# Kernel optimization log

Hardware: AMD Instinct MI355X
Metric: run time of the kernel (lower is better)

## Reference

```python
import jax, jax.numpy as jnp
import numpy as np

N, E, FX, H, B = 50000, 800000, 64, 64, 8
EPS = 1e-5


def _bn(h, gamma, beta):
    # BatchNorm1d in training mode: batch statistics, biased variance
    mu = h.mean(axis=0)
    var = ((h - mu) ** 2).mean(axis=0)
    return (h - mu) * jax.lax.rsqrt(var + EPS) * gamma + beta


def setup_inputs() -> dict:
    key = jax.random.key(0)
    ks = jax.random.split(key, 10)
    s = 0.05
    inp = {
        "x": jax.random.normal(ks[0], (N, FX), jnp.float32),
        "edge_index": jax.random.randint(ks[1], (2, E), 0, N),
        "edge_attr": jax.random.normal(ks[2], (E, H), jnp.float32),
        "u": jnp.zeros((1,), jnp.float32),
        "batch": jax.random.randint(ks[3], (E,), 0, B),
        # message_function params: Linear(FX+H->H), BN(H), Linear(H->H)
        "w1m": jax.random.normal(ks[4], (FX + H, H), jnp.float32) * s,
        "b1m": jnp.zeros((H,), jnp.float32),
        "gamma_m": jnp.ones((H,), jnp.float32),
        "beta_m": jnp.zeros((H,), jnp.float32),
        "w2m": jax.random.normal(ks[5], (H, H), jnp.float32) * s,
        "b2m": jnp.zeros((H,), jnp.float32),
        # node_mlp params: Linear(FX+H->H), BN(H), Linear(H->H)
        "w1n": jax.random.normal(ks[6], (FX + H, H), jnp.float32) * s,
        "b1n": jnp.zeros((H,), jnp.float32),
        "gamma_n": jnp.ones((H,), jnp.float32),
        "beta_n": jnp.zeros((H,), jnp.float32),
        "w2n": jax.random.normal(ks[7], (H, H), jnp.float32) * s,
        "b2n": jnp.zeros((H,), jnp.float32),
    }
    return inp


def reference(x, edge_index, edge_attr, u, batch,
              w1m, b1m, gamma_m, beta_m, w2m, b2m,
              w1n, b1n, gamma_n, beta_n, w2n, b2n):
    send_idx, rec_idx = edge_index[0], edge_index[1]
    n = x.shape[0]
    # gather sender node features, concat with edge features: [E, FX+H]
    m = jnp.concatenate([x[send_idx], edge_attr], axis=1)
    # message MLP: Linear -> BN -> ReLU -> Linear
    m = jax.nn.relu(_bn(m @ w1m + b1m, gamma_m, beta_m)) @ w2m + b2m
    # scatter_mean over receiving node index
    sums = jax.ops.segment_sum(m, rec_idx, num_segments=n)
    cnt = jax.ops.segment_sum(jnp.ones((m.shape[0],), m.dtype), rec_idx, num_segments=n)
    agg = sums / jnp.maximum(cnt, 1.0)[:, None]
    # node MLP on [x, aggregated messages]
    h = jnp.concatenate([x, agg], axis=1)
    return jax.nn.relu(_bn(h @ w1n + b1n, gamma_n, beta_n)) @ w2n + b2n
```

## Files before the change

### kernel.cpp

```cpp
#include <hip/hip_runtime.h>

typedef unsigned short bfu;
typedef unsigned int u32;
typedef __attribute__((ext_vector_type(8))) short bf16x8;
typedef __attribute__((ext_vector_type(4))) float f32x4;

#define N_NODES 50000
#define N_EDGES 800000
#define EPS_BN 1e-5f

__device__ __forceinline__ float bf2f(bfu u) { union { u32 i; float f; } v; v.i = ((u32)u) << 16; return v.f; }
__device__ __forceinline__ bfu f2bf(float f) {
    union { float f; u32 i; } v; v.f = f;
    u32 r = v.i + 0x7FFF + ((v.i >> 16) & 1);
    return (bfu)(r >> 16);
}
template<bool BF> __device__ __forceinline__ float ldf(const void* p, int i) {
    return BF ? bf2f(((const bfu*)p)[i]) : ((const float*)p)[i];
}

__global__ void k_detect(const void* gamma, int* flag) {
    if (blockIdx.x == 0 && threadIdx.x == 0)
        *flag = (((const bfu*)gamma)[0] != 0) ? 1 : 0;
}

__global__ void k_sent(u32* out, int n) {
    int i = blockIdx.x * blockDim.x + threadIdx.x;
    if (i < n) out[i] = 0x40E040E0u;
}

__global__ void k_zero(float* p, int n) {
    int i = blockIdx.x * blockDim.x + threadIdx.x;
    if (i < n) p[i] = 0.f;
}

__global__ void k_count(const int* __restrict__ rec, float* __restrict__ cnt, int n) {
    int i = blockIdx.x * blockDim.x + threadIdx.x;
    if (i < n) atomicAdd(&cnt[rec[i]], 1.0f);
}

template<bool BF>
__global__ void k_bnfin(const float* __restrict__ sum, const float* __restrict__ sq,
                        const void* __restrict__ gamma, const void* __restrict__ beta,
                        float* __restrict__ sc, float* __restrict__ sh, float count,
                        const int* __restrict__ flag) {
    if (*flag != (BF ? 1 : 0)) return;
    int c = threadIdx.x;
    float mu  = sum[c] / count;
    float var = sq[c] / count - mu * mu;
    float s = ldf<BF>(gamma, c) * rsqrtf(var + EPS_BN);
    sc[c] = s;
    sh[c] = ldf<BF>(beta, c) - mu * s;
}

__device__ __forceinline__ void split_arr(const float f[8], bf16x8& hi, bf16x8& lo) {
#pragma unroll
    for (int j = 0; j < 8; ++j) {
        union { float f; u32 i; } v; v.f = f[j];
        hi[j] = (short)(v.i >> 16);
        union { u32 i; float f; } hf; hf.i = v.i & 0xFFFF0000u;
        float r = f[j] - hf.f;
        lo[j] = (short)f2bf(r);
    }
}
__device__ __forceinline__ void split8(const float* __restrict__ p, bf16x8& hi, bf16x8& lo) {
    float4 u = *(const float4*)p;
    float4 v = *(const float4*)(p + 4);
    float f[8] = {u.x, u.y, u.z, u.w, v.x, v.y, v.z, v.w};
    split_arr(f, hi, lo);
}

__device__ __forceinline__ void load_bfrags_f32(const float* __restrict__ wf, int l, int g,
                                                bf16x8 bhi[4][4], bf16x8 blo[4][4]) {
#pragma unroll
    for (int kt = 0; kt < 4; ++kt)
#pragma unroll
        for (int nt = 0; nt < 4; ++nt) {
            float f[8];
#pragma unroll
            for (int j = 0; j < 8; ++j)
                f[j] = wf[(kt * 32 + g * 8 + j) * 64 + nt * 16 + l];
            split_arr(f, bhi[kt][nt], blo[kt][nt]);
        }
}
__device__ __forceinline__ void load_bfrags2_f32(const float* __restrict__ wf, int l, int g,
                                                 bf16x8 bhi[2][4], bf16x8 blo[2][4]) {
#pragma unroll
    for (int kt = 0; kt < 2; ++kt)
#pragma unroll
        for (int nt = 0; nt < 4; ++nt) {
            float f[8];
#pragma unroll
            for (int j = 0; j < 8; ++j)
                f[j] = wf[(kt * 32 + g * 8 + j) * 64 + nt * 16 + l];
            split_arr(f, bhi[kt][nt], blo[kt][nt]);
        }
}

__device__ __forceinline__ void edge_tile_f32s(const float* __restrict__ xf,
                                               const float* __restrict__ eaf,
                                               int e0, int my_snd, int l, int g,
                                               const bf16x8 bhi[4][4], const bf16x8 blo[4][4],
                                               f32x4 acc[4][4]) {
#pragma unroll
    for (int mt = 0; mt < 4; ++mt)
#pragma unroll
        for (int nt = 0; nt < 4; ++nt) acc[mt][nt] = (f32x4){0.f, 0.f, 0.f, 0.f};

#pragma unroll
    for (int kt = 0; kt < 4; ++kt) {
#pragma unroll
        for (int mt = 0; mt < 4; ++mt) {
            const int row = mt * 16 + l;
            const float* src;
            if (kt < 2) {
                const int snd = __shfl(my_snd, row);
                src = xf + (size_t)snd * 64 + kt * 32 + g * 8;
            } else {
                src = eaf + (size_t)(e0 + row) * 64 + (kt - 2) * 32 + g * 8;
            }
            bf16x8 ah, al;
            split8(src, ah, al);
#pragma unroll
            for (int nt = 0; nt < 4; ++nt) {
                acc[mt][nt] = __builtin_amdgcn_mfma_f32_16x16x32_bf16(ah, bhi[kt][nt], acc[mt][nt], 0, 0, 0);
                acc[mt][nt] = __builtin_amdgcn_mfma_f32_16x16x32_bf16(al, bhi[kt][nt], acc[mt][nt], 0, 0, 0);
                acc[mt][nt] = __builtin_amdgcn_mfma_f32_16x16x32_bf16(ah, blo[kt][nt], acc[mt][nt], 0, 0, 0);
            }
        }
    }
}

__global__ __launch_bounds__(256, 2) void k_stats_edge_f32s(
    const void* __restrict__ x, const int* __restrict__ send, const void* __restrict__ ea,
    const void* __restrict__ w1, const void* __restrict__ b1,
    float* __restrict__ colsum, float* __restrict__ colsq, const int* __restrict__ flag)
{
    if (*flag != 0) return;
    const int lane = threadIdx.x & 63;
    const int l = lane & 15, g = lane >> 4;
    const int wid = (blockIdx.x * blockDim.x + threadIdx.x) >> 6;
    const int nw  = (gridDim.x * blockDim.x) >> 6;
    const float* xf  = (const float*)x;
    const float* eaf = (const float*)ea;
    const float* b1f = (const float*)b1;

    bf16x8 bhi[4][4], blo[4][4];
    load_bfrags_f32((const float*)w1, l, g, bhi, blo);
    float bias[4];
#pragma unroll
    for (int nt = 0; nt < 4; ++nt) bias[nt] = b1f[nt * 16 + l];

    float sacc[4] = {0.f, 0.f, 0.f, 0.f}, qacc[4] = {0.f, 0.f, 0.f, 0.f};

    for (int t = wid; t < N_EDGES / 64; t += nw) {
        const int e0 = t * 64;
        const int my_snd = send[e0 + lane];
        f32x4 acc[4][4];
        edge_tile_f32s(xf, eaf, e0, my_snd, l, g, bhi, blo, acc);
#pragma unroll
        for (int nt = 0; nt < 4; ++nt) {
            float s = 0.f, q = 0.f;
#pragma unroll
            for (int mt = 0; mt < 4; ++mt)
#pragma unroll
                for (int r = 0; r < 4; ++r) {
                    float h = acc[mt][nt][r] + bias[nt];
                    s += h; q += h * h;
                }
            sacc[nt] += s; qacc[nt] += q;
        }
    }
#pragma unroll
    for (int nt = 0; nt < 4; ++nt) {
        float s = sacc[nt], q = qacc[nt];
        s += __shfl_xor(s, 16); s += __shfl_xor(s, 32);
        q += __shfl_xor(q, 16); q += __shfl_xor(q, 32);
        if (g == 0) {
            atomicAdd(&colsum[nt * 16 + l], s);
            atomicAdd(&colsq [nt * 16 + l], q);
        }
    }
}

__global__ __launch_bounds__(256, 2) void k_edge2_f32s(
    const void* __restrict__ x, const int* __restrict__ send, const int* __restrict__ rec,
    const void* __restrict__ ea, const void* __restrict__ w1, const void* __restrict__ b1,
    const float* __restrict__ sc, const float* __restrict__ sh,
    float* __restrict__ pagg, const int* __restrict__ flag)
{
    if (*flag != 0) return;
    const int lane = threadIdx.x & 63;
    const int l = lane & 15, g = lane >> 4;
    const int wid = (blockIdx.x * blockDim.x + threadIdx.x) >> 6;
    const int nw  = (gridDim.x * blockDim.x) >> 6;
    const float* xf  = (const float*)x;
    const float* eaf = (const float*)ea;
    const float* b1f = (const float*)b1;

    bf16x8 bhi[4][4], blo[4][4];
    load_bfrags_f32((const float*)w1, l, g, bhi, blo);
    float scl[4], shb[4];
#pragma unroll
    for (int nt = 0; nt < 4; ++nt) {
        const int c = nt * 16 + l;
        scl[nt] = sc[c];
        shb[nt] = b1f[c] * scl[nt] + sh[c];
    }

    for (int t = wid; t < N_EDGES / 64; t += nw) {
        const int e0 = t * 64;
        const int my_snd = send[e0 + lane];
        const int my_rv  = rec [e0 + lane];
        f32x4 acc[4][4];
        edge_tile_f32s(xf, eaf, e0, my_snd, l, g, bhi, blo, acc);
#pragma unroll
        for (int mt = 0; mt < 4; ++mt)
#pragma unroll
            for (int r = 0; r < 4; ++r) {
                const int m  = mt * 16 + g * 4 + r;
                const int rv = __shfl(my_rv, m);
                float* dst = pagg + (size_t)rv * 64 + l;
#pragma unroll
                for (int nt = 0; nt < 4; ++nt) {
                    float p = fmaxf(acc[mt][nt][r] * scl[nt] + shb[nt], 0.f);
                    atomicAdd(dst + nt * 16, p);
                }
            }
    }
}

__global__ __launch_bounds__(256, 2) void k_agg_f32s(
    float* __restrict__ pagg, const float* __restrict__ cnt,
    const void* __restrict__ w2, const void* __restrict__ b2, const int* __restrict__ flag)
{
    if (*flag != 0) return;
    const int lane = threadIdx.x & 63;
    const int l = lane & 15, g = lane >> 4;
    const int wid = (blockIdx.x * blockDim.x + threadIdx.x) >> 6;
    const int nw  = (gridDim.x * blockDim.x) >> 6;
    const float* b2f = (const float*)b2;

    bf16x8 bhi[2][4], blo[2][4];
    load_bfrags2_f32((const float*)w2, l, g, bhi, blo);
    float b2l[4];
#pragma unroll
    for (int nt = 0; nt < 4; ++nt) b2l[nt] = b2f[nt * 16 + l];

    const int ntiles = (N_NODES + 63) / 64;
    for (int t = wid; t < ntiles; t += nw) {
        const int v0 = t * 64;
        f32x4 acc[4][4];
#pragma unroll
        for (int mt = 0; mt < 4; ++mt)
#pragma unroll
            for (int nt = 0; nt < 4; ++nt) acc[mt][nt] = (f32x4){0.f, 0.f, 0.f, 0.f};
#pragma unroll
        for (int kt = 0; kt < 2; ++kt) {
#pragma unroll
            for (int mt = 0; mt < 4; ++mt) {
                int v = v0 + mt * 16 + l;
                if (v >= N_NODES) v = N_NODES - 1;
                bf16x8 ah, al;
                split8(pagg + (size_t)v * 64 + kt * 32 + g * 8, ah, al);
#pragma unroll
                for (int nt = 0; nt < 4; ++nt) {
                    acc[mt][nt] = __builtin_amdgcn_mfma_f32_16x16x32_bf16(ah, bhi[kt][nt], acc[mt][nt], 0, 0, 0);
                    acc[mt][nt] = __builtin_amdgcn_mfma_f32_16x16x32_bf16(al, bhi[kt][nt], acc[mt][nt], 0, 0, 0);
                    acc[mt][nt] = __builtin_amdgcn_mfma_f32_16x16x32_bf16(ah, blo[kt][nt], acc[mt][nt], 0, 0, 0);
                }
            }
        }
#pragma unroll
        for (int mt = 0; mt < 4; ++mt)
#pragma unroll
            for (int r = 0; r < 4; ++r) {
                const int v = v0 + mt * 16 + g * 4 + r;
                if (v < N_NODES) {
                    const float c = cnt[v];
                    const float inv = 1.0f / fmaxf(c, 1.0f);
#pragma unroll
                    for (int nt = 0; nt < 4; ++nt)
                        pagg[(size_t)v * 64 + nt * 16 + l] = (acc[mt][nt][r] + c * b2l[nt]) * inv;
                }
            }
    }
}

__global__ __launch_bounds__(256, 2) void k_h_node_f32s(
    const void* __restrict__ x, const float* __restrict__ agg,
    const void* __restrict__ w1, const void* __restrict__ b1,
    float* __restrict__ hbuf,
    float* __restrict__ colsum, float* __restrict__ colsq, const int* __restrict__ flag)
{
    if (*flag != 0) return;
    const int lane = threadIdx.x & 63;
    const int l = lane & 15, g = lane >> 4;
    const int wid = (blockIdx.x * blockDim.x + threadIdx.x) >> 6;
    const int nw  = (gridDim.x * blockDim.x) >> 6;
    const float* xf  = (const float*)x;
    const float* b1f = (const float*)b1;

    bf16x8 bhi[4][4], blo[4][4];
    load_bfrags_f32((const float*)w1, l, g, bhi, blo);
    float bias[4];
#pragma unroll
    for (int nt = 0; nt < 4; ++nt) bias[nt] = b1f[nt * 16 + l];

    float sacc[4] = {0.f, 0.f, 0.f, 0.f}, qacc[4] = {0.f, 0.f, 0.f, 0.f};
    const int ntiles = (N_NODES + 63) / 64;

    for (int t = wid; t < ntiles; t += nw) {
        const int v0 = t * 64;
        f32x4 acc[4][4];
#pragma unroll
        for (int mt = 0; mt < 4; ++mt)
#pragma unroll
            for (int nt = 0; nt < 4; ++nt) acc[mt][nt] = (f32x4){0.f, 0.f, 0.f, 0.f};
#pragma unroll
        for (int kt = 0; kt < 4; ++kt) {
#pragma unroll
            for (int mt = 0; mt < 4; ++mt) {
                int v = v0 + mt * 16 + l;
                if (v >= N_NODES) v = N_NODES - 1;
                const float* src = (kt < 2)
                    ? xf  + (size_t)v * 64 + kt * 32 + g * 8
                    : agg + (size_t)v * 64 + (kt - 2) * 32 + g * 8;
                bf16x8 ah, al;
                split8(src, ah, al);
#pragma unroll
                for (int nt = 0; nt < 4; ++nt) {
                    acc[mt][nt] = __builtin_amdgcn_mfma_f32_16x16x32_bf16(ah, bhi[kt][nt], acc[mt][nt], 0, 0, 0);
                    acc[mt][nt] = __builtin_amdgcn_mfma_f32_16x16x32_bf16(al, bhi[kt][nt], acc[mt][nt], 0, 0, 0);
                    acc[mt][nt] = __builtin_amdgcn_mfma_f32_16x16x32_bf16(ah, blo[kt][nt], acc[mt][nt], 0, 0, 0);
                }
            }
        }
#pragma unroll
        for (int nt = 0; nt < 4; ++nt) {
            float s = 0.f, q = 0.f;
#pragma unroll
            for (int mt = 0; mt < 4; ++mt)
#pragma unroll
                for (int r = 0; r < 4; ++r) {
                    const int v = v0 + mt * 16 + g * 4 + r;
                    if (v < N_NODES) {
                        float h = acc[mt][nt][r] + bias[nt];
                        s += h; q += h * h;
                        hbuf[(size_t)v * 64 + nt * 16 + l] = h;
                    }
                }
            sacc[nt] += s; qacc[nt] += q;
        }
    }
#pragma unroll
    for (int nt = 0; nt < 4; ++nt) {
        float s = sacc[nt], q = qacc[nt];
        s += __shfl_xor(s, 16); s += __shfl_xor(s, 32);
        q += __shfl_xor(q, 16); q += __shfl_xor(q, 32);
        if (g == 0) {
            atomicAdd(&colsum[nt * 16 + l], s);
            atomicAdd(&colsq [nt * 16 + l], q);
        }
    }
}

__global__ __launch_bounds__(256) void k_out2_f32(
    const void* __restrict__ w2, const void* __restrict__ b2,
    const float* __restrict__ sc, const float* __restrict__ sh,
    float* __restrict__ out, const int* __restrict__ flag)
{
    if (*flag != 0) return;
    __shared__ float wlds[64 * 64];
    for (int i = threadIdx.x; i < 64 * 64; i += 256) wlds[i] = ((const float*)w2)[i];
    __syncthreads();

    const int lane = threadIdx.x & 63;
    const int wid = (blockIdx.x * blockDim.x + threadIdx.x) >> 6;
    const int nw  = (gridDim.x * blockDim.x) >> 6;
    const float scl = sc[lane], shl = sh[lane];
    const float b2l = ((const float*)b2)[lane];

    for (int v = wid; v < N_NODES; v += nw) {
        const float h1 = out[(size_t)v * 64 + lane];
        const float h  = fmaxf(h1 * scl + shl, 0.f);
        float res = b2l;
#pragma unroll
        for (int k = 0; k < 64; ++k) res += __shfl(h, k) * wlds[k * 64 + lane];
        out[(size_t)v * 64 + lane] = res;
    }
}

__device__ __forceinline__ void load_bfrags(const bfu* w1w, int l, int g, bf16x8 bfr[4][4]) {
#pragma unroll
    for (int kt = 0; kt < 4; ++kt)
#pragma unroll
        for (int nt = 0; nt < 4; ++nt) {
            bf16x8 v;
#pragma unroll
            for (int j = 0; j < 8; ++j)
                v[j] = (short)w1w[(kt * 32 + g * 8 + j) * 64 + nt * 16 + l];
            bfr[kt][nt] = v;
        }
}

__device__ __forceinline__ void edge_tile_mfma(const bfu* xw, const bfu* eaw,
                                               int e0, int my_snd, int l, int g,
                                               const bf16x8 bfr[4][4], f32x4 acc[4][4]) {
#pragma unroll
    for (int mt = 0; mt < 4; ++mt)
#pragma unroll
        for (int nt = 0; nt < 4; ++nt) acc[mt][nt] = (f32x4){0.f, 0.f, 0.f, 0.f};

#pragma unroll
    for (int kt = 0; kt < 4; ++kt) {
        bf16x8 afr[4];
#pragma unroll
        for (int mt = 0; mt < 4; ++mt) {
            const int row = mt * 16 + l;
            if (kt < 2) {
                const int snd = __shfl(my_snd, row);
                afr[mt] = *(const bf16x8*)(xw + (size_t)snd * 64 + kt * 32 + g * 8);
            } else {
                afr[mt] = *(const bf16x8*)(eaw + (size_t)(e0 + row) * 64 + (kt - 2) * 32 + g * 8);
            }
        }
#pragma unroll
        for (int mt = 0; mt < 4; ++mt)
#pragma unroll
            for (int nt = 0; nt < 4; ++nt)
                acc[mt][nt] = __builtin_amdgcn_mfma_f32_16x16x32_bf16(
                    afr[mt], bfr[kt][nt], acc[mt][nt], 0, 0, 0);
    }
}

__global__ __launch_bounds__(256) void k_stats_edge_mfma(
    const void* __restrict__ x, const int* __restrict__ send, const void* __restrict__ ea,
    const void* __restrict__ w1, const void* __restrict__ b1,
    float* __restrict__ colsum, float* __restrict__ colsq, const int* __restrict__ flag)
{
    if (*flag != 1) return;
    const int lane = threadIdx.x & 63;
    const int l = lane & 15, g = lane >> 4;
    const int wid = (blockIdx.x * blockDim.x + threadIdx.x) >> 6;
    const int nw  = (gridDim.x * blockDim.x) >> 6;
    const bfu* xw  = (const bfu*)x;
    const bfu* eaw = (const bfu*)ea;

    bf16x8 bfr[4][4];
    load_bfrags((const bfu*)w1, l, g, bfr);
    float bias[4];
#pragma unroll
    for (int nt = 0; nt < 4; ++nt) bias[nt] = bf2f(((const bfu*)b1)[nt * 16 + l]);

    float sacc[4] = {0.f, 0.f, 0.f, 0.f}, qacc[4] = {0.f, 0.f, 0.f, 0.f};

    for (int t = wid; t < N_EDGES / 64; t += nw) {
        const int e0 = t * 64;
        const int my_snd = send[e0 + lane];
        f32x4 acc[4][4];
        edge_tile_mfma(xw, eaw, e0, my_snd, l, g, bfr, acc);
#pragma unroll
        for (int nt = 0; nt < 4; ++nt) {
            float s = 0.f, q = 0.f;
#pragma unroll
            for (int mt = 0; mt < 4; ++mt)
#pragma unroll
                for (int r = 0; r < 4; ++r) {
                    float h = acc[mt][nt][r] + bias[nt];
                    s += h; q += h * h;
                }
            sacc[nt] += s; qacc[nt] += q;
        }
    }
#pragma unroll
    for (int nt = 0; nt < 4; ++nt) {
        float s = sacc[nt], q = qacc[nt];
        s += __shfl_xor(s, 16); s += __shfl_xor(s, 32);
        q += __shfl_xor(q, 16); q += __shfl_xor(q, 32);
        if (g == 0) {
            atomicAdd(&colsum[nt * 16 + l], s);
            atomicAdd(&colsq [nt * 16 + l], q);
        }
    }
}

__global__ __launch_bounds__(256) void k_edge2_mfma(
    const void* __restrict__ x, const int* __restrict__ send, const int* __restrict__ rec,
    const void* __restrict__ ea, const void* __restrict__ w1, const void* __restrict__ b1,
    const float* __restrict__ sc, const float* __restrict__ sh,
    float* __restrict__ pagg, const int* __restrict__ flag)
{
    if (*flag != 1) return;
    const int lane = threadIdx.x & 63;
    const int l = lane & 15, g = lane >> 4;
    const int wid = (blockIdx.x * blockDim.x + threadIdx.x) >> 6;
    const int nw  = (gridDim.x * blockDim.x) >> 6;
    const bfu* xw  = (const bfu*)x;
    const bfu* eaw = (const bfu*)ea;

    bf16x8 bfr[4][4];
    load_bfrags((const bfu*)w1, l, g, bfr);
    float scl[4], shb[4];
#pragma unroll
    for (int nt = 0; nt < 4; ++nt) {
        const int c = nt * 16 + l;
        const float bias = bf2f(((const bfu*)b1)[c]);
        scl[nt] = sc[c];
        shb[nt] = bias * scl[nt] + sh[c];
    }

    for (int t = wid; t < N_EDGES / 64; t += nw) {
        const int e0 = t * 64;
        const int my_snd = send[e0 + lane];
        const int my_rv  = rec [e0 + lane];
        f32x4 acc[4][4];
        edge_tile_mfma(xw, eaw, e0, my_snd, l, g, bfr, acc);
#pragma unroll
        for (int mt = 0; mt < 4; ++mt)
#pragma unroll
            for (int r = 0; r < 4; ++r) {
                const int m  = mt * 16 + g * 4 + r;
                const int rv = __shfl(my_rv, m);
                float* dst = pagg + (size_t)rv * 64 + l;
#pragma unroll
                for (int nt = 0; nt < 4; ++nt) {
                    float p = fmaxf(acc[mt][nt][r] * scl[nt] + shb[nt], 0.f);
                    atomicAdd(dst + nt * 16, p);
                }
            }
    }
}

template<bool BF>
__global__ __launch_bounds__(256) void k_agg(
    float* __restrict__ pagg, const float* __restrict__ cnt,
    const void* __restrict__ w2, const void* __restrict__ b2, const int* __restrict__ flag)
{
    if (*flag != (BF ? 1 : 0)) return;
    __shared__ float wlds[64 * 64];
    for (int i = threadIdx.x; i < 64 * 64; i += 256) wlds[i] = ldf<BF>(w2, i);
    __syncthreads();

    const int lane = threadIdx.x & 63;
    const int wid = (blockIdx.x * blockDim.x + threadIdx.x) >> 6;
    const int nw  = (gridDim.x * blockDim.x) >> 6;
    const float b = ldf<BF>(b2, lane);

    for (int v = wid; v < N_NODES; v += nw) {
        float acc = 0.f;
#pragma unroll 8
        for (int k = 0; k < 64; ++k) acc += pagg[v * 64 + k] * wlds[k * 64 + lane];
        const float c = cnt[v];
        pagg[v * 64 + lane] = (acc + c * b) / fmaxf(c, 1.0f);
    }
}

template<bool BF>
__global__ __launch_bounds__(256) void k_stats_node(
    const void* __restrict__ x, const float* __restrict__ agg,
    const void* __restrict__ w1, const void* __restrict__ b1,
    float* __restrict__ colsum, float* __restrict__ colsq, const int* __restrict__ flag)
{
    if (*flag != (BF ? 1 : 0)) return;
    __shared__ float wlds[128 * 64];
    for (int i = threadIdx.x; i < 128 * 64; i += 256) wlds[i] = ldf<BF>(w1, i);
    __syncthreads();

    const int lane = threadIdx.x & 63;
    const int wid = (blockIdx.x * blockDim.x + threadIdx.x) >> 6;
    const int nw  = (gridDim.x * blockDim.x) >> 6;
    const float bias = ldf<BF>(b1, lane);

    float sacc = 0.f, qacc = 0.f;
    for (int v = wid; v < N_NODES; v += nw) {
        float acc = bias;
#pragma unroll 8
        for (int k = 0; k < 64; ++k) acc += ldf<BF>(x, v * 64 + k) * wlds[k * 64 + lane];
#pragma unroll 8
        for (int k = 0; k < 64; ++k) acc += agg[v * 64 + k] * wlds[(64 + k) * 64 + lane];
        sacc += acc;
        qacc += acc * acc;
    }
    atomicAdd(&colsum[lane], sacc);
    atomicAdd(&colsq[lane], qacc);
}

template<bool BF>
__global__ __launch_bounds__(256) void k_out(
    const void* __restrict__ x, const float* __restrict__ agg,
    const void* __restrict__ w1, const void* __restrict__ b1,
    const void* __restrict__ w2, const void* __restrict__ b2,
    const float* __restrict__ sc, const float* __restrict__ sh,
    void* __restrict__ out, const int* __restrict__ flag)
{
    if (*flag != (BF ? 1 : 0)) return;
    __shared__ float w1lds[128 * 64];
    __shared__ float w2lds[64 * 64];
    for (int i = threadIdx.x; i < 128 * 64; i += 256) w1lds[i] = ldf<BF>(w1, i);
    for (int i = threadIdx.x; i < 64 * 64; i += 256)  w2lds[i] = ldf<BF>(w2, i);
    __syncthreads();

    const int lane = threadIdx.x & 63;
    const int wid = (blockIdx.x * blockDim.x + threadIdx.x) >> 6;
    const int nw  = (gridDim.x * blockDim.x) >> 6;
    const float bias = ldf<BF>(b1, lane);
    const float b2l  = ldf<BF>(b2, lane);
    const float scl = sc[lane], shl = sh[lane];

    for (int v = wid; v < N_NODES; v += nw) {
        float acc = bias;
#pragma unroll 8
        for (int k = 0; k < 64; ++k) acc += ldf<BF>(x, v * 64 + k) * w1lds[k * 64 + lane];
#pragma unroll 8
        for (int k = 0; k < 64; ++k) acc += agg[v * 64 + k] * w1lds[(64 + k) * 64 + lane];
        const float h = fmaxf(acc * scl + shl, 0.f);
        float res = b2l;
#pragma unroll 8
        for (int k = 0; k < 64; ++k) res += __shfl(h, k) * w2lds[k * 64 + lane];
        if (BF) ((bfu*)out)[v * 64 + lane] = f2bf(res);
        else    ((float*)out)[v * 64 + lane] = res;
    }
}

extern "C" __attribute__((visibility("default")))
void kernel_launch(void* const* d_in, const int* in_sizes, int n_in,
                   void* d_out, int out_size, void* d_ws, size_t ws_size,
                   hipStream_t stream)
{
    const void* x   = d_in[0];
    const int*  ei  = (const int*)d_in[1];
    const void* ea  = d_in[2];
    const void* w1m = d_in[5];
    const void* b1m = d_in[6];
    const void* gm  = d_in[7];
    const void* bm  = d_in[8];
    const void* w2m = d_in[9];
    const void* b2m = d_in[10];
    const void* w1n = d_in[11];
    const void* b1n = d_in[12];
    const void* gn  = d_in[13];
    const void* bn_ = d_in[14];
    const void* w2n = d_in[15];
    const void* b2n = d_in[16];

    char* ws = (char*)d_ws;
    float* pagg = (float*)(ws);
    float* cnt  = (float*)(ws + 12800000);
    float* st   = (float*)(ws + 13000000);
    int*   flag = (int*)(ws + 13002048);
    float* sum_m = st,       *sq_m = st + 64,  *sum_n = st + 128, *sq_n = st + 192;
    float* sc_m  = st + 256, *sh_m = st + 320, *sc_n  = st + 384, *sh_n = st + 448;

    const int* send = ei;
    const int* rec  = ei + N_EDGES;

    k_detect<<<1, 64, 0, stream>>>(gm, flag);
    const int nsent = out_size / 2;
    k_sent<<<(nsent + 255) / 256, 256, 0, stream>>>((u32*)d_out, nsent);
    const int zn = 3200000 + 50000 + 512;
    k_zero<<<(zn + 255) / 256, 256, 0, stream>>>(pagg, zn);
    k_count<<<(N_EDGES + 255) / 256, 256, 0, stream>>>(rec, cnt, N_EDGES);

    k_stats_edge_mfma<<<512, 256, 0, stream>>>(x, send, ea, w1m, b1m, sum_m, sq_m, flag);
    k_stats_edge_f32s<<<1563, 256, 0, stream>>>(x, send, ea, w1m, b1m, sum_m, sq_m, flag);
    k_bnfin<true ><<<1, 64, 0, stream>>>(sum_m, sq_m, gm, bm, sc_m, sh_m, (float)N_EDGES, flag);
    k_bnfin<false><<<1, 64, 0, stream>>>(sum_m, sq_m, gm, bm, sc_m, sh_m, (float)N_EDGES, flag);
    k_edge2_mfma<<<512, 256, 0, stream>>>(x, send, rec, ea, w1m, b1m, sc_m, sh_m, pagg, flag);
    k_edge2_f32s<<<1563, 256, 0, stream>>>(x, send, rec, ea, w1m, b1m, sc_m, sh_m, pagg, flag);
    k_agg<true ><<<256, 256, 0, stream>>>(pagg, cnt, w2m, b2m, flag);
    k_agg_f32s<<<196, 256, 0, stream>>>(pagg, cnt, w2m, b2m, flag);
    k_stats_node<true ><<<256, 256, 0, stream>>>(x, pagg, w1n, b1n, sum_n, sq_n, flag);
    k_h_node_f32s<<<196, 256, 0, stream>>>(x, pagg, w1n, b1n, (float*)d_out, sum_n, sq_n, flag);
    k_bnfin<true ><<<1, 64, 0, stream>>>(sum_n, sq_n, gn, bn_, sc_n, sh_n, (float)N_NODES, flag);
    k_bnfin<false><<<1, 64, 0, stream>>>(sum_n, sq_n, gn, bn_, sc_n, sh_n, (float)N_NODES, flag);
    k_out<true ><<<256, 256, 0, stream>>>(x, pagg, w1n, b1n, w2n, b2n, sc_n, sh_n, d_out, flag);
    k_out2_f32<<<256, 256, 0, stream>>>(w2n, b2n, sc_n, sh_n, (float*)d_out, flag);
}
```

Baseline: 847.9 us.

## Stage split bf16 weight fragments in LDS to raise edge kernel occupancy

The two fp32 edge kernels now convert W1 into hi/lo bf16 fragments once per block and stage them in shared memory, instead of holding 32 fragment vectors in registers per thread. The MFMA loop reads the B fragments from LDS. Launch bounds rise from 2 to 4 blocks per SM and the grids shrink to 1024 blocks, aiming for more waves in flight to hide gather latency. This adds 32 KB of LDS per block, an LDS read per MFMA group, and a per-block staging pass with a barrier.

```diff
diff --git a/kernel.cpp b/kernel.cpp
--- a/kernel.cpp
+++ b/kernel.cpp
@@ -53,14 +53,17 @@
     sh[c] = ldf<BF>(beta, c) - mu * s;
 }
 
+__device__ __forceinline__ void split1(float f, bfu& hi, bfu& lo) {
+    union { float f; u32 i; } v; v.f = f;
+    hi = (bfu)(v.i >> 16);
+    union { u32 i; float f; } hf; hf.i = v.i & 0xFFFF0000u;
+    lo = f2bf(f - hf.f);
+}
 __device__ __forceinline__ void split_arr(const float f[8], bf16x8& hi, bf16x8& lo) {
 #pragma unroll
     for (int j = 0; j < 8; ++j) {
-        union { float f; u32 i; } v; v.f = f[j];
-        hi[j] = (short)(v.i >> 16);
-        union { u32 i; float f; } hf; hf.i = v.i & 0xFFFF0000u;
-        float r = f[j] - hf.f;
-        lo[j] = (short)f2bf(r);
+        bfu h, l2; split1(f[j], h, l2);
+        hi[j] = (short)h; lo[j] = (short)l2;
     }
 }
 __device__ __forceinline__ void split8(const float* __restrict__ p, bf16x8& hi, bf16x8& lo) {
@@ -97,46 +100,33 @@
         }
 }
 
-__device__ __forceinline__ void edge_tile_f32s(const float* __restrict__ xf,
-                                               const float* __restrict__ eaf,
-                                               int e0, int my_snd, int l, int g,
-                                               const bf16x8 bhi[4][4], const bf16x8 blo[4][4],
-                                               f32x4 acc[4][4]) {
-#pragma unroll
-    for (int mt = 0; mt < 4; ++mt)
-#pragma unroll
-        for (int nt = 0; nt < 4; ++nt) acc[mt][nt] = (f32x4){0.f, 0.f, 0.f, 0.f};
-
-#pragma unroll
-    for (int kt = 0; kt < 4; ++kt) {
-#pragma unroll
-        for (int mt = 0; mt < 4; ++mt) {
-            const int row = mt * 16 + l;
-            const float* src;
-            if (kt < 2) {
-                const int snd = __shfl(my_snd, row);
-                src = xf + (size_t)snd * 64 + kt * 32 + g * 8;
-            } else {
-                src = eaf + (size_t)(e0 + row) * 64 + (kt - 2) * 32 + g * 8;
-            }
-            bf16x8 ah, al;
-            split8(src, ah, al);
-#pragma unroll
-            for (int nt = 0; nt < 4; ++nt) {
-                acc[mt][nt] = __builtin_amdgcn_mfma_f32_16x16x32_bf16(ah, bhi[kt][nt], acc[mt][nt], 0, 0, 0);
-                acc[mt][nt] = __builtin_amdgcn_mfma_f32_16x16x32_bf16(al, bhi[kt][nt], acc[mt][nt], 0, 0, 0);
-                acc[mt][nt] = __builtin_amdgcn_mfma_f32_16x16x32_bf16(ah, blo[kt][nt], acc[mt][nt], 0, 0, 0);
-            }
-        }
-    }
-}
-
-__global__ __launch_bounds__(256, 2) void k_stats_edge_f32s(
+__device__ __forceinline__ void stage_wfrags_lds(const float* __restrict__ wf,
+                                                 bfu* __restrict__ whi, bfu* __restrict__ wlo,
+                                                 int tid) {
+    for (int idx = tid; idx < 8192; idx += 256) {
+        const int j  = idx & 7;
+        const int ln = (idx >> 3) & 63;
+        const int nt = (idx >> 9) & 3;
+        const int kt = idx >> 11;
+        const int l = ln & 15, g = ln >> 4;
+        bfu h, lo;
+        split1(wf[(kt * 32 + g * 8 + j) * 64 + nt * 16 + l], h, lo);
+        whi[idx] = h; wlo[idx] = lo;
+    }
+}
+
+
+__global__ __launch_bounds__(256, 4) void k_stats_edge_f32s(
     const void* __restrict__ x, const int* __restrict__ send, const void* __restrict__ ea,
     const void* __restrict__ w1, const void* __restrict__ b1,
     float* __restrict__ colsum, float* __restrict__ colsq, const int* __restrict__ flag)
 {
     if (*flag != 0) return;
+    __shared__ __align__(16) bfu whi[8192];
+    __shared__ __align__(16) bfu wlo[8192];
+    stage_wfrags_lds((const float*)w1, whi, wlo, threadIdx.x);
+    __syncthreads();
+
     const int lane = threadIdx.x & 63;
     const int l = lane & 15, g = lane >> 4;
     const int wid = (blockIdx.x * blockDim.x + threadIdx.x) >> 6;
@@ -145,8 +135,6 @@
     const float* eaf = (const float*)ea;
     const float* b1f = (const float*)b1;
 
-    bf16x8 bhi[4][4], blo[4][4];
-    load_bfrags_f32((const float*)w1, l, g, bhi, blo);
     float bias[4];
 #pragma unroll
     for (int nt = 0; nt < 4; ++nt) bias[nt] = b1f[nt * 16 + l];
@@ -157,7 +145,31 @@
         const int e0 = t * 64;
         const int my_snd = send[e0 + lane];
         f32x4 acc[4][4];
-        edge_tile_f32s(xf, eaf, e0, my_snd, l, g, bhi, blo, acc);
+#pragma unroll
+        for (int mt = 0; mt < 4; ++mt)
+#pragma unroll
+            for (int nt = 0; nt < 4; ++nt) acc[mt][nt] = (f32x4){0.f, 0.f, 0.f, 0.f};
+
+#pragma unroll
+        for (int kt = 0; kt < 4; ++kt) {
+#pragma unroll
+            for (int mt = 0; mt < 4; ++mt) {
+                const int row = mt * 16 + l;
+                const float* src = (kt < 2)
+                    ? xf  + (size_t)__shfl(my_snd, row) * 64 + kt * 32 + g * 8
+                    : eaf + (size_t)(e0 + row) * 64 + (kt - 2) * 32 + g * 8;
+                bf16x8 ah, al;
+                split8(src, ah, al);
+#pragma unroll
+                for (int nt = 0; nt < 4; ++nt) {
+                    const bf16x8 bh = *(const bf16x8*)(whi + ((kt * 4 + nt) * 64 + lane) * 8);
+                    const bf16x8 bl = *(const bf16x8*)(wlo + ((kt * 4 + nt) * 64 + lane) * 8);
+                    acc[mt][nt] = __builtin_amdgcn_mfma_f32_16x16x32_bf16(ah, bh, acc[mt][nt], 0, 0, 0);
+                    acc[mt][nt] = __builtin_amdgcn_mfma_f32_16x16x32_bf16(al, bh, acc[mt][nt], 0, 0, 0);
+                    acc[mt][nt] = __builtin_amdgcn_mfma_f32_16x16x32_bf16(ah, bl, acc[mt][nt], 0, 0, 0);
+                }
+            }
+        }
 #pragma unroll
         for (int nt = 0; nt < 4; ++nt) {
             float s = 0.f, q = 0.f;
@@ -183,13 +195,18 @@
     }
 }
 
-__global__ __launch_bounds__(256, 2) void k_edge2_f32s(
+__global__ __launch_bounds__(256, 4) void k_edge2_f32s(
     const void* __restrict__ x, const int* __restrict__ send, const int* __restrict__ rec,
     const void* __restrict__ ea, const void* __restrict__ w1, const void* __restrict__ b1,
     const float* __restrict__ sc, const float* __restrict__ sh,
     float* __restrict__ pagg, const int* __restrict__ flag)
 {
     if (*flag != 0) return;
+    __shared__ __align__(16) bfu whi[8192];
+    __shared__ __align__(16) bfu wlo[8192];
+    stage_wfrags_lds((const float*)w1, whi, wlo, threadIdx.x);
+    __syncthreads();
+
     const int lane = threadIdx.x & 63;
     const int l = lane & 15, g = lane >> 4;
     const int wid = (blockIdx.x * blockDim.x + threadIdx.x) >> 6;
@@ -198,8 +215,6 @@
     const float* eaf = (const float*)ea;
     const float* b1f = (const float*)b1;
 
-    bf16x8 bhi[4][4], blo[4][4];
-    load_bfrags_f32((const float*)w1, l, g, bhi, blo);
     float scl[4], shb[4];
 #pragma unroll
     for (int nt = 0; nt < 4; ++nt) {
@@ -213,7 +228,31 @@
         const int my_snd = send[e0 + lane];
         const int my_rv  = rec [e0 + lane];
         f32x4 acc[4][4];
-        edge_tile_f32s(xf, eaf, e0, my_snd, l, g, bhi, blo, acc);
+#pragma unroll
+        for (int mt = 0; mt < 4; ++mt)
+#pragma unroll
+            for (int nt = 0; nt < 4; ++nt) acc[mt][nt] = (f32x4){0.f, 0.f, 0.f, 0.f};
+
+#pragma unroll
+        for (int kt = 0; kt < 4; ++kt) {
+#pragma unroll
+            for (int mt = 0; mt < 4; ++mt) {
+                const int row = mt * 16 + l;
+                const float* src = (kt < 2)
+                    ? xf  + (size_t)__shfl(my_snd, row) * 64 + kt * 32 + g * 8
+                    : eaf + (size_t)(e0 + row) * 64 + (kt - 2) * 32 + g * 8;
+                bf16x8 ah, al;
+                split8(src, ah, al);
+#pragma unroll
+                for (int nt = 0; nt < 4; ++nt) {
+                    const bf16x8 bh = *(const bf16x8*)(whi + ((kt * 4 + nt) * 64 + lane) * 8);
+                    const bf16x8 bl = *(const bf16x8*)(wlo + ((kt * 4 + nt) * 64 + lane) * 8);
+                    acc[mt][nt] = __builtin_amdgcn_mfma_f32_16x16x32_bf16(ah, bh, acc[mt][nt], 0, 0, 0);
+                    acc[mt][nt] = __builtin_amdgcn_mfma_f32_16x16x32_bf16(al, bh, acc[mt][nt], 0, 0, 0);
+                    acc[mt][nt] = __builtin_amdgcn_mfma_f32_16x16x32_bf16(ah, bl, acc[mt][nt], 0, 0, 0);
+                }
+            }
+        }
 #pragma unroll
         for (int mt = 0; mt < 4; ++mt)
 #pragma unroll
@@ -663,11 +702,11 @@
     k_count<<<(N_EDGES + 255) / 256, 256, 0, stream>>>(rec, cnt, N_EDGES);
 
     k_stats_edge_mfma<<<512, 256, 0, stream>>>(x, send, ea, w1m, b1m, sum_m, sq_m, flag);
-    k_stats_edge_f32s<<<1563, 256, 0, stream>>>(x, send, ea, w1m, b1m, sum_m, sq_m, flag);
+    k_stats_edge_f32s<<<1024, 256, 0, stream>>>(x, send, ea, w1m, b1m, sum_m, sq_m, flag);
     k_bnfin<true ><<<1, 64, 0, stream>>>(sum_m, sq_m, gm, bm, sc_m, sh_m, (float)N_EDGES, flag);
     k_bnfin<false><<<1, 64, 0, stream>>>(sum_m, sq_m, gm, bm, sc_m, sh_m, (float)N_EDGES, flag);
     k_edge2_mfma<<<512, 256, 0, stream>>>(x, send, rec, ea, w1m, b1m, sc_m, sh_m, pagg, flag);
-    k_edge2_f32s<<<1563, 256, 0, stream>>>(x, send, rec, ea, w1m, b1m, sc_m, sh_m, pagg, flag);
+    k_edge2_f32s<<<1024, 256, 0, stream>>>(x, send, rec, ea, w1m, b1m, sc_m, sh_m, pagg, flag);
     k_agg<true ><<<256, 256, 0, stream>>>(pagg, cnt, w2m, b2m, flag);
     k_agg_f32s<<<196, 256, 0, stream>>>(pagg, cnt, w2m, b2m, flag);
     k_stats_node<true ><<<256, 256, 0, stream>>>(x, pagg, w1n, b1n, sum_n, sq_n, flag);
```

Measured after the change: 964.9 us. +13.8%, slower.
